# Optimization experiments

Hardware: AMD Instinct MI355X
Metric: run time of the kernel (lower is better)

The kernel has to match this reference:

```python
import jax, jax.numpy as jnp
import numpy as np

B, Cfi, H, W = 2, 32, 192, 192
Cfp, Cfo, NUM = 1, 2, 16
N = H * W
Ct = Cfo + Cfi + Cfi + Cfp  # 67
EPS = 1e-5


def _bn(x, g, b, m, v):
    # x: (B, C, num, N); per-channel inference batchnorm
    inv = g * jax.lax.rsqrt(v + EPS)
    return x * inv[None, :, None, None] + (b - m * inv)[None, :, None, None]


def _pconv(x, Wt):
    # 1x1 conv as channel contraction: Wt (Cout, Cin), x (B, Cin, num, N)
    return jnp.einsum('oc,bcmn->bomn', Wt, x)


def setup_inputs() -> dict:
    key = jax.random.key(0)
    ks = jax.random.split(key, 32)
    inp = {
        'If': jax.random.normal(ks[0], (B, Cfi, H, W), jnp.float32),
        'Pf': jax.random.normal(ks[1], (B, Cfp, H, W), jnp.float32),
        'Ofnum': jax.random.normal(ks[2], (B, Cfo, NUM, N), jnp.float32),
        'args': jax.random.randint(ks[3], (B, NUM, N), 0, N, jnp.int64),
    }
    def conv_w(k, co, ci):
        return jax.random.normal(k, (co, ci), jnp.float32) * (1.0 / np.sqrt(ci))
    def bn_p(k, c):
        k1, k2 = jax.random.split(k)
        return (jnp.ones((c,), jnp.float32),
                jnp.zeros((c,), jnp.float32),
                jax.random.normal(k1, (c,), jnp.float32) * 0.1,
                jax.random.uniform(k2, (c,), jnp.float32, 0.5, 1.5))
    # convXF: Ct->Cfi, Cfi->Cfi (both BN+GELU)
    inp['W1'] = conv_w(ks[4], Cfi, Ct)
    inp['g1'], inp['b1'], inp['m1'], inp['v1'] = bn_p(ks[5], Cfi)
    inp['W2'] = conv_w(ks[6], Cfi, Cfi)
    inp['g2'], inp['b2'], inp['m2'], inp['v2'] = bn_p(ks[7], Cfi)
    # convXL: Cfi->Cfi (BN+GELU), Cfi->Cfi (BN only)
    inp['W3'] = conv_w(ks[8], Cfi, Cfi)
    inp['g3'], inp['b3'], inp['m3'], inp['v3'] = bn_p(ks[9], Cfi)
    inp['W4'] = conv_w(ks[10], Cfi, Cfi)
    inp['g4'], inp['b4'], inp['m4'], inp['v4'] = bn_p(ks[11], Cfi)
    # coef: Cfi -> 3, with bias
    inp['Wc'] = conv_w(ks[12], 3, Cfi)
    inp['bc'] = jax.random.normal(ks[13], (3,), jnp.float32) * 0.01
    return inp


def reference(If, Pf, Ofnum, args,
              W1, g1, b1, m1, v1,
              W2, g2, b2, m2, v2,
              W3, g3, b3, m3, v3,
              W4, g4, b4, m4, v4,
              Wc, bc):
    gelu = lambda x: jax.nn.gelu(x, approximate=False)
    If_flat = If.reshape(B, Cfi, N)   # (B, Cfi, N)
    Pf_flat = Pf.reshape(B, Cfp, N)   # (B, Cfp, M), M == N here

    # per-batch neighbor gather along flattened spatial dim
    gath = jax.vmap(lambda f, a: f[:, a])  # (C,N),(num,N) -> (C,num,N)
    IPfnum = gath(If_flat, args)            # (B, Cfi, num, N)
    Pfnum = gath(Pf_flat, args)             # (B, Cfp, num, N)
    Ifnum = jnp.broadcast_to(If_flat[:, :, None, :], (B, Cfi, NUM, N))

    X = jnp.concatenate([Ifnum, IPfnum, Pfnum, Ofnum], axis=1)  # (B, Ct, num, N)

    h = gelu(_bn(_pconv(X, W1), g1, b1, m1, v1))
    h = gelu(_bn(_pconv(h, W2), g2, b2, m2, v2))
    l = gelu(_bn(_pconv(h, W3), g3, b3, m3, v3))
    l = _bn(_pconv(l, W4), g4, b4, m4, v4)
    XF = gelu(h + l)

    feat = _pconv(XF, Wc) + bc[None, :, None, None]  # (B, 3, num, N)
    Alpha, Beta, Omega = feat[:, 0:1], feat[:, 1:2], feat[:, 2:3]
    Omega = jax.nn.softmax(Omega, axis=2)
    dout = jnp.sum(((Alpha + 1.0) * Pfnum[:, -1:] + Beta) * Omega,
                   axis=2, keepdims=True)  # (B, 1, 1, N)
    return dout.reshape(B, 1, H, W)
```

## Files before the change

### kernel.cpp

```cpp
#include <hip/hip_runtime.h>
#include <math.h>

#define BB   2
#define CFI  32
#define NN   36864
#define NUMM 16

#define ZOFS (BB * NN * CFI)

typedef __attribute__((ext_vector_type(8))) short short8;
typedef __attribute__((ext_vector_type(4))) float f4;
typedef __attribute__((ext_vector_type(16))) float f16v;

static __device__ __forceinline__ f16v mm32(short8 a, short8 b, f16v c) {
    return __builtin_amdgcn_mfma_f32_32x32x16_bf16(a, b, c, 0, 0, 0);
}

template <int CTRL>
static __device__ __forceinline__ float dpp_add(float x) {
    int y = __builtin_amdgcn_update_dpp(0, __builtin_bit_cast(int, x),
                                        CTRL, 0xf, 0xf, true);
    return x + __builtin_bit_cast(float, y);
}
template <int CTRL>
static __device__ __forceinline__ float dpp_max(float x) {
    int y = __builtin_amdgcn_update_dpp(0, __builtin_bit_cast(int, x),
                                        CTRL, 0xf, 0xf, true);
    return fmaxf(x, __builtin_bit_cast(float, y));
}

static __device__ __forceinline__ float gelu_fast(float x) {
    const float x2  = x * x;
    const float q   = fmaf(-0.10294310f, x2, -2.30211813f);
    const float e   = exp2f(q * x);
    const float r   = __builtin_amdgcn_rcpf(e + 1.0f);
    return x * r;
}

static __device__ __forceinline__ unsigned bf16_rne_bits(float x) {
    unsigned u = __builtin_bit_cast(unsigned, x);
    return u + 0x7fffu + ((u >> 16) & 1u);
}
static __device__ __forceinline__ void split_pack(float x0, float x1,
                                                  unsigned& hi, unsigned& lo) {
    unsigned r0 = bf16_rne_bits(x0);
    unsigned r1 = bf16_rne_bits(x1);
    float h0 = __builtin_bit_cast(float, r0 & 0xffff0000u);
    float h1 = __builtin_bit_cast(float, r1 & 0xffff0000u);
    hi = (r0 >> 16) | (r1 & 0xffff0000u);
    unsigned s0 = bf16_rne_bits(x0 - h0);
    unsigned s1 = bf16_rne_bits(x1 - h1);
    lo = (s0 >> 16) | (s1 & 0xffff0000u);
}

static __device__ __forceinline__ unsigned pack2(float a, float b) {
    unsigned ua = __builtin_bit_cast(unsigned, a) + 0x8000u;
    unsigned ub = __builtin_bit_cast(unsigned, b) + 0x8000u;
    return (ua >> 16) | (ub & 0xffff0000u);
}

union UV { unsigned u[4]; short8 v; };

__global__ __launch_bounds__(256) void yz_kernel(
    const float* __restrict__ If, const float* __restrict__ Pf,
    const float* __restrict__ W1, const float* __restrict__ g1,
    const float* __restrict__ b1, const float* __restrict__ m1,
    const float* __restrict__ v1,
    float* __restrict__ wsYZ)
{
    __shared__ float wy[1024], wz[1024], wp[32], bt1[32];
    for (int i = threadIdx.x; i < 1024; i += 256) {
        int o = i >> 5, c = i & 31;
        float inv = g1[o] * rsqrtf(v1[o] + 1e-5f);
        wy[i] = W1[o * 67 + c]      * inv;
        wz[i] = W1[o * 67 + 32 + c] * inv;
    }
    if (threadIdx.x < 32) {
        int o = threadIdx.x;
        float inv = g1[o] * rsqrtf(v1[o] + 1e-5f);
        wp[o]  = W1[o * 67 + 64] * inv;
        bt1[o] = b1[o] - m1[o] * inv;
    }
    __syncthreads();

    const int r  = threadIdx.x & 3;
    const int p  = blockIdx.x * 64 + (threadIdx.x >> 2);
    const int b  = p / NN, n = p - b * NN;
    const int o0 = r * 8;
    const float* ifp = If + (size_t)b * CFI * NN + n;

    float v[32];
#pragma unroll
    for (int c = 0; c < 32; c++) v[c] = ifp[(size_t)c * NN];
    const float pf = Pf[p];

    float accY[8], accZ[8];
#pragma unroll
    for (int j = 0; j < 8; j++) {
        const float4* wyr = (const float4*)&wy[(o0 + j) * 32];
        const float4* wzr = (const float4*)&wz[(o0 + j) * 32];
        float ay = bt1[o0 + j];
        float az = wp[o0 + j] * pf;
#pragma unroll
        for (int c4 = 0; c4 < 8; c4++) {
            float4 a = wyr[c4], z = wzr[c4];
            ay = fmaf(a.x, v[4 * c4 + 0], ay);  az = fmaf(z.x, v[4 * c4 + 0], az);
            ay = fmaf(a.y, v[4 * c4 + 1], ay);  az = fmaf(z.y, v[4 * c4 + 1], az);
            ay = fmaf(a.z, v[4 * c4 + 2], ay);  az = fmaf(z.z, v[4 * c4 + 2], az);
            ay = fmaf(a.w, v[4 * c4 + 3], ay);  az = fmaf(z.w, v[4 * c4 + 3], az);
        }
        accY[j] = ay; accZ[j] = az;
    }

    float4* yp = (float4*)(wsYZ + (size_t)p * 32 + o0);
    float4* zp = (float4*)(wsYZ + ZOFS + (size_t)p * 32 + o0);
    yp[0] = make_float4(accY[0], accY[1], accY[2], accY[3]);
    yp[1] = make_float4(accY[4], accY[5], accY[6], accY[7]);
    zp[0] = make_float4(accZ[0], accZ[1], accZ[2], accZ[3]);
    zp[1] = make_float4(accZ[4], accZ[5], accZ[6], accZ[7]);
}

#define LOADL(Lc)                                                             \
    {                                                                         \
        A0l = *(const short8*)&wfrag[(Lc)][0][1][lane + io][0];               \
        A0h = *(const short8*)&wfrag[(Lc)][0][0][lane + io][0];               \
        A1l = *(const short8*)&wfrag[(Lc)][1][1][lane + io][0];               \
        A1h = *(const short8*)&wfrag[(Lc)][1][0][lane + io][0];               \
        bq0 = *(const f4*)&btl[(Lc) * 32 +      4 * hi + 4 * io];             \
        bq1 = *(const f4*)&btl[(Lc) * 32 +  8 + 4 * hi + 4 * io];             \
        bq2 = *(const f4*)&btl[(Lc) * 32 + 16 + 4 * hi + 4 * io];             \
        bq3 = *(const f4*)&btl[(Lc) * 32 + 24 + 4 * hi + 4 * io];             \
    }

#define LAYER_MM(ACCV, BIN0, BIN1)                                            \
    {                                                                         \
        ACCV[0]  = bq0[0]; ACCV[1]  = bq0[1]; ACCV[2]  = bq0[2]; ACCV[3]  = bq0[3]; \
        ACCV[4]  = bq1[0]; ACCV[5]  = bq1[1]; ACCV[6]  = bq1[2]; ACCV[7]  = bq1[3]; \
        ACCV[8]  = bq2[0]; ACCV[9]  = bq2[1]; ACCV[10] = bq2[2]; ACCV[11] = bq2[3]; \
        ACCV[12] = bq3[0]; ACCV[13] = bq3[1]; ACCV[14] = bq3[2]; ACCV[15] = bq3[3]; \
        ACCV = mm32(A0l, BIN0.v, ACCV);                                       \
        ACCV = mm32(A0h, BIN0.v, ACCV);                                       \
        ACCV = mm32(A1l, BIN1.v, ACCV);                                       \
        ACCV = mm32(A1h, BIN1.v, ACCV);                                       \
    }

#define RELAYOUT(SRC, B0V, B1V)                                               \
    {                                                                         \
        B0V.u[0] = pack2(SRC[0],  SRC[1]);                                    \
        B0V.u[1] = pack2(SRC[2],  SRC[3]);                                    \
        B0V.u[2] = pack2(SRC[4],  SRC[5]);                                    \
        B0V.u[3] = pack2(SRC[6],  SRC[7]);                                    \
        B1V.u[0] = pack2(SRC[8],  SRC[9]);                                    \
        B1V.u[1] = pack2(SRC[10], SRC[11]);                                   \
        B1V.u[2] = pack2(SRC[12], SRC[13]);                                   \
        B1V.u[3] = pack2(SRC[14], SRC[15]);                                   \
    }

__global__ __launch_bounds__(256, 4) void main_kernel(
    const float* __restrict__ Pf, const float* __restrict__ Of,
    const int* __restrict__ args,
    const float* __restrict__ W1, const float* __restrict__ g1,
    const float* __restrict__ v1,
    const float* __restrict__ W2, const float* __restrict__ g2,
    const float* __restrict__ b2, const float* __restrict__ m2,
    const float* __restrict__ v2,
    const float* __restrict__ W3, const float* __restrict__ g3,
    const float* __restrict__ b3, const float* __restrict__ m3,
    const float* __restrict__ v3,
    const float* __restrict__ W4, const float* __restrict__ g4,
    const float* __restrict__ b4, const float* __restrict__ m4,
    const float* __restrict__ v4,
    const float* __restrict__ Wc, const float* __restrict__ bc,
    const float* __restrict__ ws, float* __restrict__ out)
{
    __shared__ __align__(16) unsigned wfrag[3][2][2][64][4];
    __shared__ __align__(16) float btl[3 * 32];
    __shared__ __align__(16) float wch[3 * 32];
    __shared__ __align__(16) float w1t[2 * 32];
    __shared__ float bcs[3];
    __shared__ int   izs;

    const float* Ws[3] = {W2, W3, W4};
    const float* gs[3] = {g2, g3, g4};
    const float* vs[3] = {v2, v3, v4};
    const float* bs[3] = {b2, b3, b4};
    const float* ms[3] = {m2, m3, m4};

    for (int idx = threadIdx.x; idx < 1536; idx += 256) {
        int pp  = idx & 3;
        int ln  = (idx >> 2) & 63;
        int kh  = (idx >> 8) & 1;
        int L   = idx >> 9;
        int row = ln & 31;
        int g   = ln >> 5;
        int k   = kh * 16 + 4 * g + 2 * (pp & 1) + 8 * (pp >> 1);
        float inv = gs[L][row] * rsqrtf(vs[L][row] + 1e-5f);
        float w0 = Ws[L][row * 32 + k]     * inv;
        float w1 = Ws[L][row * 32 + k + 1] * inv;
        unsigned hiw, low;
        split_pack(w0, w1, hiw, low);
        wfrag[L][kh][0][ln][pp] = hiw;
        wfrag[L][kh][1][ln][pp] = low;
    }
    if (threadIdx.x < 96) {
        int L = threadIdx.x >> 5, ch = threadIdx.x & 31;
        btl[threadIdx.x] = bs[L][ch] - ms[L][ch] * (gs[L][ch] * rsqrtf(vs[L][ch] + 1e-5f));
        wch[threadIdx.x] = Wc[L * 32 + ch];
    }
    if (threadIdx.x < 64) {
        int t = threadIdx.x >> 5, ch = threadIdx.x & 31;
        float i1 = g1[ch] * rsqrtf(v1[ch] + 1e-5f);
        w1t[threadIdx.x] = W1[ch * 67 + 65 + t] * i1;
    }
    if (threadIdx.x < 3) bcs[threadIdx.x] = bc[threadIdx.x];
    if (threadIdx.x == 0) izs = (int)(args[0] >> 16);
    __syncthreads();

    const int lane  = threadIdx.x & 63;
    const int wid   = threadIdx.x >> 6;
    const int m     = lane & 15;
    const int pt    = (lane >> 4) & 1;
    const int hi    = lane >> 5;
    const int q4    = hi << 2;
    const int izero = izs;

    const int base  = blockIdx.x * 32 + wid * 8 + pt;

    f4 y0, y1, y2, y3, z0, z1, z2, z3;
    float of0v, of1v, pfg_n;
    int   aI_n;
    {
        const int C0 = base;
        const int b0 = (C0 >= NN) ? 1 : 0;
        const int n0 = C0 - b0 * NN;
        const int a0 = args[(b0 * NUMM + m) * NN + n0];
        of0v = Of[((b0 * 2 + 0) * NUMM + m) * NN + n0];
        of1v = Of[((b0 * 2 + 1) * NUMM + m) * NN + n0];
        pfg_n = Pf[b0 * NN + a0];
        const f4* yb = (const f4*)(ws + (size_t)(b0 * NN + n0) * 32);
        const f4* zb = (const f4*)(ws + ZOFS + (size_t)(b0 * NN + a0) * 32);
        y0 = yb[hi]; y1 = yb[2 + hi]; y2 = yb[4 + hi]; y3 = yb[6 + hi];
        z0 = zb[hi]; z1 = zb[2 + hi]; z2 = zb[4 + hi]; z3 = zb[6 + hi];
        const int C1 = (C0 + 2 < BB * NN) ? C0 + 2 : BB * NN - 1;
        const int b1_ = (C1 >= NN) ? 1 : 0;
        const int n1_ = C1 - b1_ * NN;
        aI_n = args[(b1_ * NUMM + m) * NN + n1_];
    }

#pragma unroll 1
    for (int i = 0; i < 4; i++) {
        const int io = i & izero;
        const int C  = base + i * 2;
        const int b  = (C >= NN) ? 1 : 0;
        const int n  = C - b * NN;
        const float pfg = pfg_n;

        short8 A0l, A0h, A1l, A1h;
        f4 bq0, bq1, bq2, bq3;
        LOADL(0);

        const f4 wa0 = *(const f4*)&w1t[q4 + 4 * io];
        const f4 wa1 = *(const f4*)&w1t[8 + q4 + 4 * io];
        const f4 wa2 = *(const f4*)&w1t[16 + q4 + 4 * io];
        const f4 wa3 = *(const f4*)&w1t[24 + q4 + 4 * io];
        const f4 wb0 = *(const f4*)&w1t[32 + q4 + 4 * io];
        const f4 wb1 = *(const f4*)&w1t[40 + q4 + 4 * io];
        const f4 wb2 = *(const f4*)&w1t[48 + q4 + 4 * io];
        const f4 wb3 = *(const f4*)&w1t[56 + q4 + 4 * io];

        float x[16];
#pragma unroll
        for (int j = 0; j < 4; j++) {
            x[j]      = fmaf(of1v, wb0[j], fmaf(of0v, wa0[j], y0[j] + z0[j]));
            x[4 + j]  = fmaf(of1v, wb1[j], fmaf(of0v, wa1[j], y1[j] + z1[j]));
            x[8 + j]  = fmaf(of1v, wb2[j], fmaf(of0v, wa2[j], y2[j] + z2[j]));
            x[12 + j] = fmaf(of1v, wb3[j], fmaf(of0v, wa3[j], y3[j] + z3[j]));
        }
#pragma unroll
        for (int j = 0; j < 16; j++) x[j] = gelu_fast(x[j]);
        UV B0, B1;
        RELAYOUT(x, B0, B1);

        const int Cn = (C + 2 < BB * NN) ? C + 2 : BB * NN - 1;
        const int bn = (Cn >= NN) ? 1 : 0;
        const int nn = Cn - bn * NN;

        f16v acc;
        LAYER_MM(acc, B0, B1);
        LOADL(1);
        float h2g[16];
#pragma unroll
        for (int r = 0; r < 16; r++) h2g[r] = gelu_fast(acc[r]);
        RELAYOUT(h2g, B0, B1);

        {
            const f4* ybn = (const f4*)(ws + (size_t)(bn * NN + nn) * 32);
            y0 = ybn[hi]; y1 = ybn[2 + hi]; y2 = ybn[4 + hi]; y3 = ybn[6 + hi];
            of0v = Of[((bn * 2 + 0) * NUMM + m) * NN + nn];
            of1v = Of[((bn * 2 + 1) * NUMM + m) * NN + nn];
        }

        LAYER_MM(acc, B0, B1);
        LOADL(2);
        float h3g[16];
#pragma unroll
        for (int r = 0; r < 16; r++) h3g[r] = gelu_fast(acc[r]);
        RELAYOUT(h3g, B0, B1);

        {
            const int aN = aI_n;
            pfg_n = Pf[bn * NN + aN];
            const f4* zbn = (const f4*)(ws + ZOFS + (size_t)(bn * NN + aN) * 32);
            z0 = zbn[hi]; z1 = zbn[2 + hi]; z2 = zbn[4 + hi]; z3 = zbn[6 + hi];
            const int Ca = (C + 4 < BB * NN) ? C + 4 : BB * NN - 1;
            const int ba = (Ca >= NN) ? 1 : 0;
            const int na = Ca - ba * NN;
            aI_n = args[(ba * NUMM + m) * NN + na];
        }

        LAYER_MM(acc, B0, B1);

        float pa = 0.0f, pb = 0.0f, po = 0.0f;
#pragma unroll
        for (int q = 0; q < 4; q++) {
            const f4 wAq = *(const f4*)&wch[      8 * q + q4 + 4 * io];
            const f4 wBq = *(const f4*)&wch[32 +  8 * q + q4 + 4 * io];
            const f4 wOq = *(const f4*)&wch[64 +  8 * q + q4 + 4 * io];
#pragma unroll
            for (int r2 = 0; r2 < 4; r2++) {
                float xf = gelu_fast(h2g[4 * q + r2] + acc[4 * q + r2]);
                pa = fmaf(wAq[r2], xf, pa);
                pb = fmaf(wBq[r2], xf, pb);
                po = fmaf(wOq[r2], xf, po);
            }
        }
        pa += __shfl_xor(pa, 32, 64);
        pb += __shfl_xor(pb, 32, 64);
        po += __shfl_xor(po, 32, 64);

        const float alpha = pa + bcs[0];
        const float beta_ = pb + bcs[1];
        const float omega = po + bcs[2];
        const float val = fmaf(alpha + 1.0f, pfg, beta_);

        float mx = dpp_max<0xB1>(omega);
        mx = dpp_max<0x4E>(mx);
        mx = dpp_max<0x141>(mx);
        mx = dpp_max<0x140>(mx);
        const float e = __expf(omega - mx);
        float S = e, T = val * e;
        S = dpp_add<0xB1>(S);   T = dpp_add<0xB1>(T);
        S = dpp_add<0x4E>(S);   T = dpp_add<0x4E>(T);
        S = dpp_add<0x141>(S);  T = dpp_add<0x141>(T);
        S = dpp_add<0x140>(S);  T = dpp_add<0x140>(T);

        if ((lane & 15) == 0 && lane < 32)
            out[b * NN + n] = T * __builtin_amdgcn_rcpf(S);
    }
}

extern "C" void kernel_launch(void* const* d_in, const int* in_sizes, int n_in,
                              void* d_out, int out_size, void* d_ws, size_t ws_size,
                              hipStream_t stream) {
    const float* If    = (const float*)d_in[0];
    const float* Pf    = (const float*)d_in[1];
    const float* Of    = (const float*)d_in[2];
    const int*   args  = (const int*)d_in[3];
    const float* W1    = (const float*)d_in[4];
    const float* g1    = (const float*)d_in[5];
    const float* b1    = (const float*)d_in[6];
    const float* m1    = (const float*)d_in[7];
    const float* v1    = (const float*)d_in[8];
    const float* W2    = (const float*)d_in[9];
    const float* g2    = (const float*)d_in[10];
    const float* b2    = (const float*)d_in[11];
    const float* m2    = (const float*)d_in[12];
    const float* v2    = (const float*)d_in[13];
    const float* W3    = (const float*)d_in[14];
    const float* g3    = (const float*)d_in[15];
    const float* b3    = (const float*)d_in[16];
    const float* m3    = (const float*)d_in[17];
    const float* v3    = (const float*)d_in[18];
    const float* W4    = (const float*)d_in[19];
    const float* g4    = (const float*)d_in[20];
    const float* b4    = (const float*)d_in[21];
    const float* m4    = (const float*)d_in[22];
    const float* v4    = (const float*)d_in[23];
    const float* Wc    = (const float*)d_in[24];
    const float* bc    = (const float*)d_in[25];

    float* ws  = (float*)d_ws;
    float* out = (float*)d_out;

    yz_kernel<<<(BB * NN) / 64, 256, 0, stream>>>(
        If, Pf, W1, g1, b1, m1, v1, ws);

    main_kernel<<<(BB * NN) / 32, 256, 0, stream>>>(
        Pf, Of, args,
        W1, g1, v1,
        W2, g2, b2, m2, v2,
        W3, g3, b3, m3, v3,
        W4, g4, b4, m4, v4,
        Wc, bc, ws, out);
}
```

Before: 226.8 us.

## Store Y/Z intermediates as bf16 and issue next-iteration gathers earlier

The precomputed per-point Y and Z projections are now written to the workspace as packed bf16 instead of fp32. This halves the bytes moved by the random gather of Z rows and the streaming read of Y rows in the main kernel. The loads for the next iteration (Y, Of, Pf, Z, args) are also grouped and issued before the first MFMA layer, giving them more time in flight. The cost is bf16 rounding of the first-layer pre-activations, a possible accuracy loss, plus a little extra unpack arithmetic.

```diff
diff --git a/kernel.cpp b/kernel.cpp
--- a/kernel.cpp
+++ b/kernel.cpp
@@ -6,11 +6,13 @@
 #define NN   36864
 #define NUMM 16
 
-#define ZOFS (BB * NN * CFI)
+#define ZOFSU (BB * NN * 16)
 
 typedef __attribute__((ext_vector_type(8))) short short8;
 typedef __attribute__((ext_vector_type(4))) float f4;
 typedef __attribute__((ext_vector_type(16))) float f16v;
+typedef __attribute__((ext_vector_type(4))) unsigned uint4v;
+typedef __attribute__((ext_vector_type(2))) unsigned u2v;
 
 static __device__ __forceinline__ f16v mm32(short8 a, short8 b, f16v c) {
     return __builtin_amdgcn_mfma_f32_32x32x16_bf16(a, b, c, 0, 0, 0);
@@ -57,6 +59,12 @@
     unsigned ua = __builtin_bit_cast(unsigned, a) + 0x8000u;
     unsigned ub = __builtin_bit_cast(unsigned, b) + 0x8000u;
     return (ua >> 16) | (ub & 0xffff0000u);
+}
+static __device__ __forceinline__ float bflo(unsigned u) {
+    return __builtin_bit_cast(float, u << 16);
+}
+static __device__ __forceinline__ float bfhi(unsigned u) {
+    return __builtin_bit_cast(float, u & 0xffff0000u);
 }
 
 union UV { unsigned u[4]; short8 v; };
@@ -112,12 +120,16 @@
         accY[j] = ay; accZ[j] = az;
     }
 
-    float4* yp = (float4*)(wsYZ + (size_t)p * 32 + o0);
-    float4* zp = (float4*)(wsYZ + ZOFS + (size_t)p * 32 + o0);
-    yp[0] = make_float4(accY[0], accY[1], accY[2], accY[3]);
-    yp[1] = make_float4(accY[4], accY[5], accY[6], accY[7]);
-    zp[0] = make_float4(accZ[0], accZ[1], accZ[2], accZ[3]);
-    zp[1] = make_float4(accZ[4], accZ[5], accZ[6], accZ[7]);
+    unsigned* wsu = (unsigned*)wsYZ;
+    u2v yA, yB, zA, zB;
+    yA[0] = pack2(accY[0], accY[1]); yA[1] = pack2(accY[2], accY[3]);
+    yB[0] = pack2(accY[4], accY[5]); yB[1] = pack2(accY[6], accY[7]);
+    zA[0] = pack2(accZ[0], accZ[1]); zA[1] = pack2(accZ[2], accZ[3]);
+    zB[0] = pack2(accZ[4], accZ[5]); zB[1] = pack2(accZ[6], accZ[7]);
+    *(u2v*)(wsu + (size_t)p * 16 + 2 * r)          = yA;
+    *(u2v*)(wsu + (size_t)p * 16 + 8 + 2 * r)      = yB;
+    *(u2v*)(wsu + ZOFSU + (size_t)p * 16 + 2 * r)     = zA;
+    *(u2v*)(wsu + ZOFSU + (size_t)p * 16 + 8 + 2 * r) = zB;
 }
 
 #define LOADL(Lc)                                                             \
@@ -216,6 +228,7 @@
     if (threadIdx.x == 0) izs = (int)(args[0] >> 16);
     __syncthreads();
 
+    const unsigned* wsu = (const unsigned*)ws;
     const int lane  = threadIdx.x & 63;
     const int wid   = threadIdx.x >> 6;
     const int m     = lane & 15;
@@ -226,7 +239,7 @@
 
     const int base  = blockIdx.x * 32 + wid * 8 + pt;
 
-    f4 y0, y1, y2, y3, z0, z1, z2, z3;
+    uint4v yu0, yu1, zu0, zu1;
     float of0v, of1v, pfg_n;
     int   aI_n;
     {
@@ -237,10 +250,10 @@
         of0v = Of[((b0 * 2 + 0) * NUMM + m) * NN + n0];
         of1v = Of[((b0 * 2 + 1) * NUMM + m) * NN + n0];
         pfg_n = Pf[b0 * NN + a0];
-        const f4* yb = (const f4*)(ws + (size_t)(b0 * NN + n0) * 32);
-        const f4* zb = (const f4*)(ws + ZOFS + (size_t)(b0 * NN + a0) * 32);
-        y0 = yb[hi]; y1 = yb[2 + hi]; y2 = yb[4 + hi]; y3 = yb[6 + hi];
-        z0 = zb[hi]; z1 = zb[2 + hi]; z2 = zb[4 + hi]; z3 = zb[6 + hi];
+        const uint4v* yb = (const uint4v*)(wsu + (size_t)(b0 * NN + n0) * 16 + hi * 8);
+        const uint4v* zb = (const uint4v*)(wsu + ZOFSU + (size_t)(b0 * NN + a0) * 16 + hi * 8);
+        yu0 = yb[0]; yu1 = yb[1];
+        zu0 = zb[0]; zu1 = zb[1];
         const int C1 = (C0 + 2 < BB * NN) ? C0 + 2 : BB * NN - 1;
         const int b1_ = (C1 >= NN) ? 1 : 0;
         const int n1_ = C1 - b1_ * NN;
@@ -259,64 +272,65 @@
         f4 bq0, bq1, bq2, bq3;
         LOADL(0);
 
-        const f4 wa0 = *(const f4*)&w1t[q4 + 4 * io];
-        const f4 wa1 = *(const f4*)&w1t[8 + q4 + 4 * io];
-        const f4 wa2 = *(const f4*)&w1t[16 + q4 + 4 * io];
-        const f4 wa3 = *(const f4*)&w1t[24 + q4 + 4 * io];
-        const f4 wb0 = *(const f4*)&w1t[32 + q4 + 4 * io];
-        const f4 wb1 = *(const f4*)&w1t[40 + q4 + 4 * io];
-        const f4 wb2 = *(const f4*)&w1t[48 + q4 + 4 * io];
-        const f4 wb3 = *(const f4*)&w1t[56 + q4 + 4 * io];
+        f4 wa[4], wb[4];
+        wa[0] = *(const f4*)&w1t[q4 + 4 * io];
+        wa[1] = *(const f4*)&w1t[8 + q4 + 4 * io];
+        wa[2] = *(const f4*)&w1t[16 + q4 + 4 * io];
+        wa[3] = *(const f4*)&w1t[24 + q4 + 4 * io];
+        wb[0] = *(const f4*)&w1t[32 + q4 + 4 * io];
+        wb[1] = *(const f4*)&w1t[40 + q4 + 4 * io];
+        wb[2] = *(const f4*)&w1t[48 + q4 + 4 * io];
+        wb[3] = *(const f4*)&w1t[56 + q4 + 4 * io];
 
         float x[16];
 #pragma unroll
-        for (int j = 0; j < 4; j++) {
-            x[j]      = fmaf(of1v, wb0[j], fmaf(of0v, wa0[j], y0[j] + z0[j]));
-            x[4 + j]  = fmaf(of1v, wb1[j], fmaf(of0v, wa1[j], y1[j] + z1[j]));
-            x[8 + j]  = fmaf(of1v, wb2[j], fmaf(of0v, wa2[j], y2[j] + z2[j]));
-            x[12 + j] = fmaf(of1v, wb3[j], fmaf(of0v, wa3[j], y3[j] + z3[j]));
+        for (int q = 0; q < 4; q++) {
+            const unsigned ya0 = (q < 2) ? yu0[2 * q]     : yu1[2 * q - 4];
+            const unsigned ya1 = (q < 2) ? yu0[2 * q + 1] : yu1[2 * q - 3];
+            const unsigned za0 = (q < 2) ? zu0[2 * q]     : zu1[2 * q - 4];
+            const unsigned za1 = (q < 2) ? zu0[2 * q + 1] : zu1[2 * q - 3];
+            x[4 * q + 0] = fmaf(of1v, wb[q][0], fmaf(of0v, wa[q][0], bflo(ya0) + bflo(za0)));
+            x[4 * q + 1] = fmaf(of1v, wb[q][1], fmaf(of0v, wa[q][1], bfhi(ya0) + bfhi(za0)));
+            x[4 * q + 2] = fmaf(of1v, wb[q][2], fmaf(of0v, wa[q][2], bflo(ya1) + bflo(za1)));
+            x[4 * q + 3] = fmaf(of1v, wb[q][3], fmaf(of0v, wa[q][3], bfhi(ya1) + bfhi(za1)));
         }
 #pragma unroll
         for (int j = 0; j < 16; j++) x[j] = gelu_fast(x[j]);
         UV B0, B1;
         RELAYOUT(x, B0, B1);
 
-        const int Cn = (C + 2 < BB * NN) ? C + 2 : BB * NN - 1;
-        const int bn = (Cn >= NN) ? 1 : 0;
-        const int nn = Cn - bn * NN;
-
-        f16v acc;
-        LAYER_MM(acc, B0, B1);
-        LOADL(1);
-        float h2g[16];
-#pragma unroll
-        for (int r = 0; r < 16; r++) h2g[r] = gelu_fast(acc[r]);
-        RELAYOUT(h2g, B0, B1);
-
         {
-            const f4* ybn = (const f4*)(ws + (size_t)(bn * NN + nn) * 32);
-            y0 = ybn[hi]; y1 = ybn[2 + hi]; y2 = ybn[4 + hi]; y3 = ybn[6 + hi];
+            const int Cn = (C + 2 < BB * NN) ? C + 2 : BB * NN - 1;
+            const int bn = (Cn >= NN) ? 1 : 0;
+            const int nn = Cn - bn * NN;
+            const uint4v* ybn = (const uint4v*)(wsu + (size_t)(bn * NN + nn) * 16 + hi * 8);
+            yu0 = ybn[0]; yu1 = ybn[1];
             of0v = Of[((bn * 2 + 0) * NUMM + m) * NN + nn];
             of1v = Of[((bn * 2 + 1) * NUMM + m) * NN + nn];
-        }
-
-        LAYER_MM(acc, B0, B1);
-        LOADL(2);
-        float h3g[16];
-#pragma unroll
-        for (int r = 0; r < 16; r++) h3g[r] = gelu_fast(acc[r]);
-        RELAYOUT(h3g, B0, B1);
-
-        {
             const int aN = aI_n;
             pfg_n = Pf[bn * NN + aN];
-            const f4* zbn = (const f4*)(ws + ZOFS + (size_t)(bn * NN + aN) * 32);
-            z0 = zbn[hi]; z1 = zbn[2 + hi]; z2 = zbn[4 + hi]; z3 = zbn[6 + hi];
+            const uint4v* zbn = (const uint4v*)(wsu + ZOFSU + (size_t)(bn * NN + aN) * 16 + hi * 8);
+            zu0 = zbn[0]; zu1 = zbn[1];
             const int Ca = (C + 4 < BB * NN) ? C + 4 : BB * NN - 1;
             const int ba = (Ca >= NN) ? 1 : 0;
             const int na = Ca - ba * NN;
             aI_n = args[(ba * NUMM + m) * NN + na];
         }
+
+        f16v acc;
+        LAYER_MM(acc, B0, B1);
+        LOADL(1);
+        float h2g[16];
+#pragma unroll
+        for (int r = 0; r < 16; r++) h2g[r] = gelu_fast(acc[r]);
+        RELAYOUT(h2g, B0, B1);
+
+        LAYER_MM(acc, B0, B1);
+        LOADL(2);
+        float h3g[16];
+#pragma unroll
+        for (int r = 0; r < 16; r++) h3g[r] = gelu_fast(acc[r]);
+        RELAYOUT(h3g, B0, B1);
 
         LAYER_MM(acc, B0, B1);
 
```

Result: no change. 226.7 us (-0.0%).
